# Performance work log

Hardware: AMD Instinct MI355X
Metric: run time of the kernel (lower is better)

## Reference

```python
import jax, jax.numpy as jnp
import numpy as np

NU, NI, NA = 100000, 50000, 5000
FEAT, H, L = 256, 128, 2
E_RATES, E_SIM, E_HAS = 1000000, 500000, 250000
SCALE = 0.05


def setup_inputs() -> dict:
    key = jax.random.key(0)
    ks = jax.random.split(key, 20)
    f32 = jnp.float32
    inp = {}
    inp["x_item_feat"] = jax.random.normal(ks[0], (NI, FEAT), f32)
    inp["user_emb"] = jax.random.normal(ks[1], (NU, H), f32) * SCALE
    inp["attr_emb"] = jax.random.normal(ks[2], (NA, H), f32) * SCALE
    inp["lin_item_W"] = jax.random.normal(ks[3], (FEAT, H), f32) * SCALE
    inp["lin_item_b"] = jnp.zeros((H,), f32)
    inp["ui_Wl"] = jax.random.normal(ks[4], (L, 4, H, H), f32) * SCALE
    inp["ui_bl"] = jnp.zeros((L, 4, H), f32)
    inp["ui_Wr"] = jax.random.normal(ks[5], (L, 4, H, H), f32) * SCALE
    inp["ii_Wl"] = jax.random.normal(ks[6], (L, 2, H, H), f32) * SCALE
    inp["ii_bl"] = jnp.zeros((L, 2, H), f32)
    inp["ii_Wr"] = jax.random.normal(ks[7], (L, 2, H, H), f32) * SCALE
    inp["ia_Wl"] = jax.random.normal(ks[8], (L, 4, H, H), f32) * SCALE
    inp["ia_bl"] = jnp.zeros((L, 4, H), f32)
    inp["ia_Wr"] = jax.random.normal(ks[9], (L, 4, H, H), f32) * SCALE
    inp["alpha"] = jnp.zeros((3,), f32)
    # edge_index rows: [src; dst], ranges per node type
    inp["edge_rates"] = jnp.stack([
        jax.random.randint(ks[10], (E_RATES,), 0, NU, jnp.int32),   # user src
        jax.random.randint(ks[11], (E_RATES,), 0, NI, jnp.int32)])  # item dst
    inp["edge_sim"] = jnp.stack([
        jax.random.randint(ks[12], (E_SIM,), 0, NI, jnp.int32),
        jax.random.randint(ks[13], (E_SIM,), 0, NI, jnp.int32)])
    inp["edge_has"] = jnp.stack([
        jax.random.randint(ks[14], (E_HAS,), 0, NI, jnp.int32),    # item src
        jax.random.randint(ks[15], (E_HAS,), 0, NA, jnp.int32)])   # attr dst
    return inp


def _sage_edge(x_src, x_dst, src, dst, Wl, bl, Wr):
    # PyG SAGEConv: lin_l(mean of neighbor messages) + lin_r(root)
    n_dst = x_dst.shape[0]
    agg = jax.ops.segment_sum(x_src[src], dst, num_segments=n_dst)
    cnt = jax.ops.segment_sum(jnp.ones(src.shape[0], x_src.dtype), dst, num_segments=n_dst)
    agg = agg / jnp.maximum(cnt, 1.0)[:, None]
    return agg @ Wl + bl + x_dst @ Wr


def _sage_self(x, Wl, bl, Wr):
    # 'self' relation realized as identity self-loops: mean aggr of single self neighbor = x
    return x @ Wl + bl + x @ Wr


def reference(x_item_feat, user_emb, attr_emb, lin_item_W, lin_item_b,
              ui_Wl, ui_bl, ui_Wr, ii_Wl, ii_bl, ii_Wr, ia_Wl, ia_bl, ia_Wr,
              alpha, edge_rates, edge_sim, edge_has):
    x_item = x_item_feat @ lin_item_W + lin_item_b
    relu = jax.nn.relu

    # user-item branch (relations: 0=rates u->i, 1=rev_rates i->u, 2=user self, 3=item self)
    hu, hi = user_emb, x_item
    for l in range(L):
        o_i = 0.5 * (_sage_edge(hu, hi, edge_rates[0], edge_rates[1], ui_Wl[l, 0], ui_bl[l, 0], ui_Wr[l, 0])
                     + _sage_self(hi, ui_Wl[l, 3], ui_bl[l, 3], ui_Wr[l, 3]))
        o_u = 0.5 * (_sage_edge(hi, hu, edge_rates[1], edge_rates[0], ui_Wl[l, 1], ui_bl[l, 1], ui_Wr[l, 1])
                     + _sage_self(hu, ui_Wl[l, 2], ui_bl[l, 2], ui_Wr[l, 2]))
        hu, hi = relu(o_u), relu(o_i)
    h_ui_item = hi

    # item-item content branch (0=sim, 1=item self)
    h = x_item
    for l in range(L):
        o = 0.5 * (_sage_edge(h, h, edge_sim[0], edge_sim[1], ii_Wl[l, 0], ii_bl[l, 0], ii_Wr[l, 0])
                   + _sage_self(h, ii_Wl[l, 1], ii_bl[l, 1], ii_Wr[l, 1]))
        h = relu(o)
    h_ii_item = h

    # item-attr branch (0=has i->a, 1=rev_has a->i, 2=item self, 3=attr self)
    hi2, ha = x_item, attr_emb
    for l in range(L):
        o_a = 0.5 * (_sage_edge(hi2, ha, edge_has[0], edge_has[1], ia_Wl[l, 0], ia_bl[l, 0], ia_Wr[l, 0])
                     + _sage_self(ha, ia_Wl[l, 3], ia_bl[l, 3], ia_Wr[l, 3]))
        o_i = 0.5 * (_sage_edge(ha, hi2, edge_has[1], edge_has[0], ia_Wl[l, 1], ia_bl[l, 1], ia_Wr[l, 1])
                     + _sage_self(hi2, ia_Wl[l, 2], ia_bl[l, 2], ia_Wr[l, 2]))
        hi2, ha = relu(o_i), relu(o_a)
    h_ia_item = hi2

    w = jax.nn.softmax(alpha)
    h_fused = w[0] * h_ui_item + w[1] * h_ii_item + w[2] * h_ia_item
    return (h_fused, h_ui_item, h_ii_item, h_ia_item, w)
```

## Files before the change

### kernel.cpp

```cpp
#include <hip/hip_runtime.h>

#define NU_ 100000
#define NI_ 50000
#define NA_ 5000
#define FEAT_ 256
#define H_ 128
#define ER_ 1000000
#define ES_ 500000
#define EH_ 250000

#define NTOT_ (3 * NI_ + NU_ + NA_)
#define RTOT_ (2 * ER_ + ES_ + 2 * EH_)
#define NSB_ ((NTOT_ + 1023) / 1024)
#define SBCAP_ 65536
#define B_RI 0
#define B_RU (NI_)
#define B_SI (NI_ + NU_)
#define B_HA (2 * NI_ + NU_)
#define B_HI (2 * NI_ + NU_ + NA_)

typedef long long i64;
typedef unsigned short u16;
typedef unsigned int u32;
typedef __attribute__((ext_vector_type(8))) short bf16x8;
typedef __attribute__((ext_vector_type(4))) float f32x4;

__device__ __forceinline__ u16 f2bf(float v) {
    u32 b = __float_as_uint(v);
    b += 0x7fff + ((b >> 16) & 1);
    return (u16)(b >> 16);
}
__device__ __forceinline__ float bf2f(u16 v) {
    return __uint_as_float((u32)v << 16);
}

__global__ __launch_bounds__(256) void tobf_kernel(const float4* __restrict__ in,
                                                   ushort4* __restrict__ out, long n4) {
    long i = (long)blockIdx.x * 256 + threadIdx.x;
    if (i >= n4) return;
    float4 v = in[i];
    ushort4 o;
    o.x = f2bf(v.x); o.y = f2bf(v.y); o.z = f2bf(v.z); o.w = f2bf(v.w);
    out[i] = o;
}

__device__ __forceinline__ void rec_of(int r, const int* __restrict__ er,
                                       const int* __restrict__ es,
                                       const int* __restrict__ eh,
                                       int& node, int& val) {
    if (r < 2 * ER_) {
        int e = r >> 1;
        if ((r & 1) == 0) { node = B_RI + er[ER_ + e]; val = er[e]; }
        else              { node = B_RU + er[e];       val = er[ER_ + e]; }
    } else if (r < 2 * ER_ + ES_) {
        int e = r - 2 * ER_;
        node = B_SI + es[ES_ + e]; val = es[e];
    } else {
        int q = r - 2 * ER_ - ES_;
        int e = q >> 1;
        if ((q & 1) == 0) { node = B_HA + eh[EH_ + e]; val = eh[e]; }
        else              { node = B_HI + eh[e];       val = eh[EH_ + e]; }
    }
}

__global__ __launch_bounds__(256) void sbinit_kernel(int* __restrict__ sbc,
                                                     int* __restrict__ OFF) {
    int t = threadIdx.x;
    sbc[t] = t << 16;
    if (t < 4) OFF[t] = 0;
}

__global__ __launch_bounds__(256) void binA_kernel(const int* __restrict__ er,
                                                   const int* __restrict__ es,
                                                   const int* __restrict__ eh,
                                                   int* __restrict__ sbc,
                                                   int* __restrict__ cpool) {
    __shared__ int h[256];
    __shared__ int gof[256];
    int t = threadIdx.x;
    h[t] = 0;
    __syncthreads();
    int base = blockIdx.x * 4096;
    int sbs[16];
    u32 recs[16];
#pragma unroll
    for (int i = 0; i < 16; ++i) {
        int r = base + i * 256 + t;
        sbs[i] = -1;
        if (r < RTOT_) {
            int node, val;
            rec_of(r, er, es, eh, node, val);
            int sb = node >> 10;
            sbs[i] = sb;
            recs[i] = ((u32)(node & 1023) << 17) | (u32)val;
            atomicAdd(&h[sb], 1);
        }
    }
    __syncthreads();
    {
        int c = h[t];
        if (c > 0) gof[t] = atomicAdd(&sbc[t], c);
        h[t] = 0;
    }
    __syncthreads();
#pragma unroll
    for (int i = 0; i < 16; ++i) {
        if (sbs[i] >= 0) {
            int slot = atomicAdd(&h[sbs[i]], 1);
            cpool[gof[sbs[i]] + slot] = (int)recs[i];
        }
    }
}

__global__ __launch_bounds__(256) void sbscan_kernel(const int* __restrict__ sbc,
                                                     int* __restrict__ sbb) {
    int t = threadIdx.x;
    int v = (t < NSB_) ? (sbc[t] - (t << 16)) : 0;
    int incl = v;
    int lane = t & 63;
#pragma unroll
    for (int d = 1; d < 64; d <<= 1) {
        int u = __shfl_up(incl, d);
        if (lane >= d) incl += u;
    }
    __shared__ int wsum[4];
    if (lane == 63) wsum[t >> 6] = incl;
    __syncthreads();
    int wo = 0;
    for (int i = 0; i < (t >> 6); ++i) wo += wsum[i];
    if (t < NSB_) sbb[t] = wo + incl - v;
}

__global__ __launch_bounds__(1024) void binB_kernel(const int* __restrict__ cpool,
                                                    const int* __restrict__ sbb,
                                                    const int* __restrict__ sbc,
                                                    int* __restrict__ off1,
                                                    int* __restrict__ pool) {
    __shared__ int c[1024];
    __shared__ int b[1024];
    __shared__ int wsum[16];
    int sb = blockIdx.x, t = threadIdx.x;
    int rlo = sb << 16, rhi = sbc[sb];
    int base = sbb[sb];
    c[t] = 0;
    __syncthreads();
    for (int j = rlo + t; j < rhi; j += 1024)
        atomicAdd(&c[((u32)cpool[j]) >> 17], 1);
    __syncthreads();
    int v = c[t];
    int incl = v;
    int lane = t & 63;
#pragma unroll
    for (int d = 1; d < 64; d <<= 1) {
        int u = __shfl_up(incl, d);
        if (lane >= d) incl += u;
    }
    if (lane == 63) wsum[t >> 6] = incl;
    __syncthreads();
    int wo = 0;
    for (int i = 0; i < (t >> 6); ++i) wo += wsum[i];
    int ex = wo + incl - v;
    int node = sb * 1024 + t;
    if (node < NTOT_) off1[node] = base + ex + v;
    b[t] = base + ex;
    __syncthreads();
    for (int j = rlo + t; j < rhi; j += 1024) {
        u32 rec = (u32)cpool[j];
        int pos = atomicAdd(&b[rec >> 17], 1);
        pool[pos] = (int)(rec & 0x1FFFF);
    }
}

#define ACC8(A, V)                                                            \
    {                                                                         \
        A[0] += bf2f((u16)(V.x & 0xffff)); A[1] += bf2f((u16)(V.x >> 16));    \
        A[2] += bf2f((u16)(V.y & 0xffff)); A[3] += bf2f((u16)(V.y >> 16));    \
        A[4] += bf2f((u16)(V.z & 0xffff)); A[5] += bf2f((u16)(V.z >> 16));    \
        A[6] += bf2f((u16)(V.w & 0xffff)); A[7] += bf2f((u16)(V.w >> 16));    \
    }

__global__ __launch_bounds__(256) void gatherb_kernel(const u16* __restrict__ feat,
                                                      const int* __restrict__ off1,
                                                      const int* __restrict__ pool,
                                                      int n,
                                                      u16* __restrict__ agg) {
    int row = blockIdx.x * 16 + (threadIdx.x >> 4);
    if (row >= n) return;
    int lane = (threadIdx.x & 15) * 8;
    int start = off1[row - 1];
    int end = off1[row];
    float a0[8], a1[8], a2[8], a3[8];
#pragma unroll
    for (int k = 0; k < 8; ++k) { a0[k] = 0.f; a1[k] = 0.f; a2[k] = 0.f; a3[k] = 0.f; }
    int j = start;
    for (; j + 4 <= end; j += 4) {
        int s0 = pool[j], s1 = pool[j + 1], s2 = pool[j + 2], s3 = pool[j + 3];
        uint4 v0 = *(const uint4*)&feat[(i64)s0 * H_ + lane];
        uint4 v1 = *(const uint4*)&feat[(i64)s1 * H_ + lane];
        uint4 v2 = *(const uint4*)&feat[(i64)s2 * H_ + lane];
        uint4 v3 = *(const uint4*)&feat[(i64)s3 * H_ + lane];
        ACC8(a0, v0); ACC8(a1, v1); ACC8(a2, v2); ACC8(a3, v3);
    }
    for (; j < end; ++j) {
        int s0 = pool[j];
        uint4 v0 = *(const uint4*)&feat[(i64)s0 * H_ + lane];
        ACC8(a0, v0);
    }
    float inv = 1.0f / fmaxf((float)(end - start), 1.0f);
    uint4 o;
    float r0, r1;
    r0 = (a0[0] + a1[0] + a2[0] + a3[0]) * inv; r1 = (a0[1] + a1[1] + a2[1] + a3[1]) * inv;
    o.x = (u32)f2bf(r0) | ((u32)f2bf(r1) << 16);
    r0 = (a0[2] + a1[2] + a2[2] + a3[2]) * inv; r1 = (a0[3] + a1[3] + a2[3] + a3[3]) * inv;
    o.y = (u32)f2bf(r0) | ((u32)f2bf(r1) << 16);
    r0 = (a0[4] + a1[4] + a2[4] + a3[4]) * inv; r1 = (a0[5] + a1[5] + a2[5] + a3[5]) * inv;
    o.z = (u32)f2bf(r0) | ((u32)f2bf(r1) << 16);
    r0 = (a0[6] + a1[6] + a2[6] + a3[6]) * inv; r1 = (a0[7] + a1[7] + a2[7] + a3[7]) * inv;
    o.w = (u32)f2bf(r0) | ((u32)f2bf(r1) << 16);
    *(uint4*)&agg[(i64)row * H_ + lane] = o;
}

struct WJob {
    const float* s0; const float* s1; const float* s2;
    int logK; int base;
};
struct WJobs { WJob j[17]; };

__global__ __launch_bounds__(256) void wsplit_kernel(WJobs jobs, int njobs, int total,
                                                     u16* __restrict__ WTH,
                                                     u16* __restrict__ WTL) {
    int gid = blockIdx.x * 256 + threadIdx.x;
    if (gid >= total) return;
    int ji = 0;
    for (int i = 1; i < 17; ++i)
        if (i < njobs && gid >= jobs.j[i].base) ji = i;
    WJob jb = jobs.j[ji];
    int local = gid - jb.base;
    int e = local & 7;
    int l = (local >> 3) & 63;
    int nt = (local >> 9) & 7;
    int kc = local >> 12;
    int n = nt * 16 + (l & 15);
    int k = kc * 32 + ((l >> 4) << 3) + e;
    i64 si = (i64)k * 128 + n;
    float v = jb.s0[si];
    if (jb.s1 != nullptr) v += jb.s1[si] + jb.s2[si];
    if (jb.logK == 8) {
        u32 b = __float_as_uint(v);
        u16 h = (u16)(b >> 16);
        float rem = v - __uint_as_float(b & 0xffff0000u);
        WTH[gid] = h;
        WTL[gid] = (u16)(__float_as_uint(rem) >> 16);
    } else {
        WTH[gid] = f2bf(v);
    }
}

__device__ __forceinline__ void split8(const float* f, bf16x8& h, bf16x8& lo) {
#pragma unroll
    for (int i = 0; i < 8; ++i) {
        u32 b = __float_as_uint(f[i]);
        h[i] = (short)(u16)(b >> 16);
        float rem = f[i] - __uint_as_float(b & 0xffff0000u);
        lo[i] = (short)(u16)(__float_as_uint(rem) >> 16);
    }
}

__global__ __launch_bounds__(256) void mgemm_x_kernel(
    const float* __restrict__ A, const u16* __restrict__ Wh, const u16* __restrict__ Wl,
    const float* __restrict__ bias, u16* __restrict__ Cbf, int M) {
    int t = threadIdx.x;
    int w = t >> 6, l = t & 63;
    int lr = l & 15, lq = l >> 4;
    int m0 = blockIdx.x * 128 + w * 32;

    f32x4 acc[2][8];
#pragma unroll
    for (int mt = 0; mt < 2; ++mt)
#pragma unroll
        for (int nt = 0; nt < 8; ++nt) acc[mt][nt] = (f32x4){0.f, 0.f, 0.f, 0.f};

    for (int kc = 0; kc < 8; ++kc) {
        bf16x8 ah0, al0, ah1, al1;
        {
            int row = m0 + lr;
            float f[8];
            if (row < M) {
                const float* ap = &A[(i64)row * FEAT_ + kc * 32 + lq * 8];
                *(float4*)&f[0] = *(const float4*)ap;
                *(float4*)&f[4] = *(const float4*)(ap + 4);
            } else {
#pragma unroll
                for (int i = 0; i < 8; ++i) f[i] = 0.f;
            }
            split8(f, ah0, al0);
        }
        {
            int row = m0 + 16 + lr;
            float f[8];
            if (row < M) {
                const float* ap = &A[(i64)row * FEAT_ + kc * 32 + lq * 8];
                *(float4*)&f[0] = *(const float4*)ap;
                *(float4*)&f[4] = *(const float4*)(ap + 4);
            } else {
#pragma unroll
                for (int i = 0; i < 8; ++i) f[i] = 0.f;
            }
            split8(f, ah1, al1);
        }
        const u16* whp = Wh + ((i64)kc * 8) * 512 + (i64)l * 8;
        const u16* wlp = Wl + ((i64)kc * 8) * 512 + (i64)l * 8;
#pragma unroll
        for (int nt = 0; nt < 8; ++nt) {
            bf16x8 bh = *(const bf16x8*)(whp + nt * 512);
            bf16x8 bl = *(const bf16x8*)(wlp + nt * 512);
            acc[0][nt] = __builtin_amdgcn_mfma_f32_16x16x32_bf16(ah0, bh, acc[0][nt], 0, 0, 0);
            acc[1][nt] = __builtin_amdgcn_mfma_f32_16x16x32_bf16(ah1, bh, acc[1][nt], 0, 0, 0);
            acc[0][nt] = __builtin_amdgcn_mfma_f32_16x16x32_bf16(al0, bh, acc[0][nt], 0, 0, 0);
            acc[1][nt] = __builtin_amdgcn_mfma_f32_16x16x32_bf16(al1, bh, acc[1][nt], 0, 0, 0);
            acc[0][nt] = __builtin_amdgcn_mfma_f32_16x16x32_bf16(ah0, bl, acc[0][nt], 0, 0, 0);
            acc[1][nt] = __builtin_amdgcn_mfma_f32_16x16x32_bf16(ah1, bl, acc[1][nt], 0, 0, 0);
        }
    }
#pragma unroll
    for (int nt = 0; nt < 8; ++nt) {
        int col = nt * 16 + lr;
        float bb = bias[col];
#pragma unroll
        for (int mt = 0; mt < 2; ++mt) {
#pragma unroll
            for (int r = 0; r < 4; ++r) {
                int row = m0 + mt * 16 + (lq << 2) + r;
                if (row < M) Cbf[(i64)row * H_ + col] = f2bf(acc[mt][nt][r] + bb);
            }
        }
    }
}

__global__ __launch_bounds__(256) void mgemm_d_kernel(
    const u16* __restrict__ A1, const u16* __restrict__ W1,
    const u16* __restrict__ A2, const u16* __restrict__ W2,
    const float* __restrict__ b1, const float* __restrict__ b2,
    float* __restrict__ C, u16* __restrict__ Cbf, int M,
    const float* __restrict__ alpha, const float* __restrict__ fu,
    const float* __restrict__ fi, float* __restrict__ fout,
    float* __restrict__ wout) {
    int t = threadIdx.x;
    int w = t >> 6, l = t & 63;
    int lr = l & 15, lq = l >> 4;
    int m0 = blockIdx.x * 128 + w * 32;

    f32x4 acc[2][8];
#pragma unroll
    for (int mt = 0; mt < 2; ++mt)
#pragma unroll
        for (int nt = 0; nt < 8; ++nt) acc[mt][nt] = (f32x4){0.f, 0.f, 0.f, 0.f};

#pragma unroll
    for (int mat = 0; mat < 2; ++mat) {
        const u16* A = mat ? A2 : A1;
        const u16* W = mat ? W2 : W1;
#pragma unroll
        for (int kc = 0; kc < 4; ++kc) {
            bf16x8 a0 = {0, 0, 0, 0, 0, 0, 0, 0}, a1 = {0, 0, 0, 0, 0, 0, 0, 0};
            int row0 = m0 + lr, row1 = m0 + 16 + lr;
            if (row0 < M) a0 = *(const bf16x8*)&A[(i64)row0 * H_ + kc * 32 + lq * 8];
            if (row1 < M) a1 = *(const bf16x8*)&A[(i64)row1 * H_ + kc * 32 + lq * 8];
            const u16* wp = W + ((i64)kc * 8) * 512 + (i64)l * 8;
#pragma unroll
            for (int nt = 0; nt < 8; ++nt) {
                bf16x8 bw = *(const bf16x8*)(wp + nt * 512);
                acc[0][nt] = __builtin_amdgcn_mfma_f32_16x16x32_bf16(a0, bw, acc[0][nt], 0, 0, 0);
                acc[1][nt] = __builtin_amdgcn_mfma_f32_16x16x32_bf16(a1, bw, acc[1][nt], 0, 0, 0);
            }
        }
    }

    float w0 = 0.f, w1 = 0.f, w2 = 0.f;
    if (fout != nullptr) {
        float x0 = alpha[0], x1 = alpha[1], x2 = alpha[2];
        float mx = fmaxf(x0, fmaxf(x1, x2));
        float e0 = __expf(x0 - mx), e1 = __expf(x1 - mx), e2 = __expf(x2 - mx);
        float inv = 1.f / (e0 + e1 + e2);
        w0 = e0 * inv; w1 = e1 * inv; w2 = e2 * inv;
        if (blockIdx.x == 0 && t == 0) { wout[0] = w0; wout[1] = w1; wout[2] = w2; }
    }

#pragma unroll
    for (int nt = 0; nt < 8; ++nt) {
        int col = nt * 16 + lr;
        float bb = 0.5f * (b1[col] + b2[col]);
#pragma unroll
        for (int mt = 0; mt < 2; ++mt) {
#pragma unroll
            for (int r = 0; r < 4; ++r) {
                int row = m0 + mt * 16 + (lq << 2) + r;
                if (row < M) {
                    i64 idx = (i64)row * H_ + col;
                    float o = fmaxf(0.5f * acc[mt][nt][r] + bb, 0.f);
                    if (C != nullptr) C[idx] = o;
                    if (Cbf != nullptr) Cbf[idx] = f2bf(o);
                    if (fout != nullptr) fout[idx] = w0 * fu[idx] + w1 * fi[idx] + w2 * o;
                }
            }
        }
    }
}

extern "C" void kernel_launch(void* const* d_in, const int* in_sizes, int n_in,
                              void* d_out, int out_size, void* d_ws, size_t ws_size,
                              hipStream_t stream) {
    const float* xif  = (const float*)d_in[0];
    const float* uemb = (const float*)d_in[1];
    const float* aemb = (const float*)d_in[2];
    const float* liW  = (const float*)d_in[3];
    const float* lib  = (const float*)d_in[4];
    const float* uiWl = (const float*)d_in[5];
    const float* uibl = (const float*)d_in[6];
    const float* uiWr = (const float*)d_in[7];
    const float* iiWl = (const float*)d_in[8];
    const float* iibl = (const float*)d_in[9];
    const float* iiWr = (const float*)d_in[10];
    const float* iaWl = (const float*)d_in[11];
    const float* iabl = (const float*)d_in[12];
    const float* iaWr = (const float*)d_in[13];
    const float* alpha = (const float*)d_in[14];
    const int* er = (const int*)d_in[15];
    const int* es = (const int*)d_in[16];
    const int* eh = (const int*)d_in[17];

    float* out = (float*)d_out;
    float* FUSED  = out;
    float* OUT_UI = out + (i64)NI_ * H_;
    float* OUT_II = out + (i64)2 * NI_ * H_;
    float* OUT_IA = out + (i64)3 * NI_ * H_;
    float* WOUT   = out + (i64)4 * NI_ * H_;

    u16* u = (u16*)d_ws;
    i64 uo = 0;
    u16* WTH    = u + uo; uo += 294912;
    u16* WTL    = u + uo; uo += 294912;
    u16* X_bf   = u + uo; uo += (i64)NI_ * H_;
    u16* HI1_bf = u + uo; uo += (i64)NI_ * H_;
    u16* HU1_bf = u + uo; uo += (i64)NU_ * H_;
    u16* HA1_bf = u + uo; uo += (i64)NA_ * H_;
    u16* AGG_bf = u + uo; uo += (i64)NU_ * H_;
    u16* UE_bf  = u + uo; uo += (i64)NU_ * H_;
    u16* AE_bf  = u + uo; uo += (i64)NA_ * H_;

    int* ip = (int*)(u + uo);
    i64 io = 0;
    int* OFF   = ip + io; io += NTOT_ + 4;
    int* SBB   = ip + io; io += 256;
    int* SBC   = ip + io; io += 256;
    int* POOL  = ip + io; io += RTOT_;
    int* CPOOL = ip + io; io += (i64)NSB_ << 16;
    int* off1 = OFF + 1;

    {
        sbinit_kernel<<<1, 256, 0, stream>>>(SBC, OFF);
        int nblk = (RTOT_ + 4095) / 4096;
        binA_kernel<<<nblk, 256, 0, stream>>>(er, es, eh, SBC, CPOOL);
        sbscan_kernel<<<1, 256, 0, stream>>>(SBC, SBB);
        binB_kernel<<<NSB_, 1024, 0, stream>>>(CPOOL, SBB, SBC, off1, POOL);
    }

    const float* famWl[8] = {uiWl, uiWl, uiWl, iiWl, iiWl, iaWl, iaWl, iaWl};
    const float* famWr[8] = {uiWr, uiWr, uiWr, iiWr, iiWr, iaWr, iaWr, iaWr};
    const float* famBl[8] = {uibl, uibl, uibl, iibl, iibl, iabl, iabl, iabl};
    const int eidx[8] = {0, 1, 4, 0, 2, 0, 1, 5};
    const int sidx[8] = {3, 2, 7, 1, 3, 3, 2, 6};

    WJobs jobs;
    jobs.j[0] = {liW, nullptr, nullptr, 8, 0};
    int base = 32768;
    for (int s = 0; s < 8; ++s) {
        jobs.j[1 + 2 * s] = {famWl[s] + (i64)eidx[s] * 16384, nullptr, nullptr, 7, base};
        base += 16384;
        jobs.j[2 + 2 * s] = {famWr[s] + (i64)eidx[s] * 16384,
                             famWl[s] + (i64)sidx[s] * 16384,
                             famWr[s] + (i64)sidx[s] * 16384, 7, base};
        base += 16384;
    }
    wsplit_kernel<<<(base + 255) / 256, 256, 0, stream>>>(jobs, 17, base, WTH, WTL);

    tobf_kernel<<<((NU_ * H_ / 4) + 255) / 256, 256, 0, stream>>>(
        (const float4*)uemb, (ushort4*)UE_bf, (long)NU_ * H_ / 4);
    tobf_kernel<<<((NA_ * H_ / 4) + 255) / 256, 256, 0, stream>>>(
        (const float4*)aemb, (ushort4*)AE_bf, (long)NA_ * H_ / 4);

    mgemm_x_kernel<<<(NI_ + 127) / 128, 256, 0, stream>>>(xif, WTH, WTL, lib, X_bf, NI_);

    auto gath = [&](const u16* feat, int cbase, int ndst) {
        gatherb_kernel<<<(ndst + 15) / 16, 256, 0, stream>>>(feat, off1 + cbase, POOL, ndst, AGG_bf);
    };
    auto gemm2 = [&](int slot, const u16* A2m, float* Cout, u16* Cbfout, int M,
                     const float* al = nullptr, const float* fu = nullptr,
                     const float* fi = nullptr, float* fo = nullptr,
                     float* wo = nullptr) {
        const u16* w1 = WTH + 32768 + (i64)(2 * slot) * 16384;
        const u16* w2 = WTH + 32768 + (i64)(2 * slot + 1) * 16384;
        const float* be = famBl[slot] + (i64)eidx[slot] * 128;
        const float* bs = famBl[slot] + (i64)sidx[slot] * 128;
        mgemm_d_kernel<<<(M + 127) / 128, 256, 0, stream>>>(
            AGG_bf, w1, A2m, w2, be, bs, Cout, Cbfout, M, al, fu, fi, fo, wo);
    };

    gath(UE_bf, B_RI, NI_);
    gemm2(0, X_bf, nullptr, HI1_bf, NI_);
    gath(X_bf, B_RU, NU_);
    gemm2(1, UE_bf, nullptr, HU1_bf, NU_);
    gath(HU1_bf, B_RI, NI_);
    gemm2(2, HI1_bf, OUT_UI, nullptr, NI_);

    gath(X_bf, B_SI, NI_);
    gemm2(3, X_bf, nullptr, HI1_bf, NI_);
    gath(HI1_bf, B_SI, NI_);
    gemm2(4, HI1_bf, OUT_II, nullptr, NI_);

    gath(X_bf, B_HA, NA_);
    gemm2(5, AE_bf, nullptr, HA1_bf, NA_);
    gath(AE_bf, B_HI, NI_);
    gemm2(6, X_bf, nullptr, HI1_bf, NI_);
    gath(HA1_bf, B_HI, NI_);
    gemm2(7, HI1_bf, OUT_IA, nullptr, NI_, alpha, OUT_UI, OUT_II, FUSED, WOUT);
}
```

Before: 549.7 us.

## Batch independent gather and GEMM stages into packed multi-op launches

Replaces the serial chain of 17 gather/GEMM kernel launches with 6 launches of a packed kernel. Each launch runs several independent operations from the three branches concurrently, and the block index is dispatched to the op it belongs to. Separate aggregation and hidden buffers per branch remove the false dependencies that the shared AGG/HI1 buffers forced. This is meant to cut launch overhead and fill the GPU during small stages. In exchange it uses more workspace memory and a single kernel with larger register pressure across the combined code paths.

```diff
diff --git a/kernel.cpp b/kernel.cpp
--- a/kernel.cpp
+++ b/kernel.cpp
@@ -12,7 +12,6 @@
 #define NTOT_ (3 * NI_ + NU_ + NA_)
 #define RTOT_ (2 * ER_ + ES_ + 2 * EH_)
 #define NSB_ ((NTOT_ + 1023) / 1024)
-#define SBCAP_ 65536
 #define B_RI 0
 #define B_RU (NI_)
 #define B_SI (NI_ + NU_)
@@ -169,55 +168,6 @@
         int pos = atomicAdd(&b[rec >> 17], 1);
         pool[pos] = (int)(rec & 0x1FFFF);
     }
-}
-
-#define ACC8(A, V)                                                            \
-    {                                                                         \
-        A[0] += bf2f((u16)(V.x & 0xffff)); A[1] += bf2f((u16)(V.x >> 16));    \
-        A[2] += bf2f((u16)(V.y & 0xffff)); A[3] += bf2f((u16)(V.y >> 16));    \
-        A[4] += bf2f((u16)(V.z & 0xffff)); A[5] += bf2f((u16)(V.z >> 16));    \
-        A[6] += bf2f((u16)(V.w & 0xffff)); A[7] += bf2f((u16)(V.w >> 16));    \
-    }
-
-__global__ __launch_bounds__(256) void gatherb_kernel(const u16* __restrict__ feat,
-                                                      const int* __restrict__ off1,
-                                                      const int* __restrict__ pool,
-                                                      int n,
-                                                      u16* __restrict__ agg) {
-    int row = blockIdx.x * 16 + (threadIdx.x >> 4);
-    if (row >= n) return;
-    int lane = (threadIdx.x & 15) * 8;
-    int start = off1[row - 1];
-    int end = off1[row];
-    float a0[8], a1[8], a2[8], a3[8];
-#pragma unroll
-    for (int k = 0; k < 8; ++k) { a0[k] = 0.f; a1[k] = 0.f; a2[k] = 0.f; a3[k] = 0.f; }
-    int j = start;
-    for (; j + 4 <= end; j += 4) {
-        int s0 = pool[j], s1 = pool[j + 1], s2 = pool[j + 2], s3 = pool[j + 3];
-        uint4 v0 = *(const uint4*)&feat[(i64)s0 * H_ + lane];
-        uint4 v1 = *(const uint4*)&feat[(i64)s1 * H_ + lane];
-        uint4 v2 = *(const uint4*)&feat[(i64)s2 * H_ + lane];
-        uint4 v3 = *(const uint4*)&feat[(i64)s3 * H_ + lane];
-        ACC8(a0, v0); ACC8(a1, v1); ACC8(a2, v2); ACC8(a3, v3);
-    }
-    for (; j < end; ++j) {
-        int s0 = pool[j];
-        uint4 v0 = *(const uint4*)&feat[(i64)s0 * H_ + lane];
-        ACC8(a0, v0);
-    }
-    float inv = 1.0f / fmaxf((float)(end - start), 1.0f);
-    uint4 o;
-    float r0, r1;
-    r0 = (a0[0] + a1[0] + a2[0] + a3[0]) * inv; r1 = (a0[1] + a1[1] + a2[1] + a3[1]) * inv;
-    o.x = (u32)f2bf(r0) | ((u32)f2bf(r1) << 16);
-    r0 = (a0[2] + a1[2] + a2[2] + a3[2]) * inv; r1 = (a0[3] + a1[3] + a2[3] + a3[3]) * inv;
-    o.y = (u32)f2bf(r0) | ((u32)f2bf(r1) << 16);
-    r0 = (a0[4] + a1[4] + a2[4] + a3[4]) * inv; r1 = (a0[5] + a1[5] + a2[5] + a3[5]) * inv;
-    o.z = (u32)f2bf(r0) | ((u32)f2bf(r1) << 16);
-    r0 = (a0[6] + a1[6] + a2[6] + a3[6]) * inv; r1 = (a0[7] + a1[7] + a2[7] + a3[7]) * inv;
-    o.w = (u32)f2bf(r0) | ((u32)f2bf(r1) << 16);
-    *(uint4*)&agg[(i64)row * H_ + lane] = o;
 }
 
 struct WJob {
@@ -256,6 +206,54 @@
     }
 }
 
+#define ACC8(A, V)                                                            \
+    {                                                                         \
+        A[0] += bf2f((u16)(V.x & 0xffff)); A[1] += bf2f((u16)(V.x >> 16));    \
+        A[2] += bf2f((u16)(V.y & 0xffff)); A[3] += bf2f((u16)(V.y >> 16));    \
+        A[4] += bf2f((u16)(V.z & 0xffff)); A[5] += bf2f((u16)(V.z >> 16));    \
+        A[6] += bf2f((u16)(V.w & 0xffff)); A[7] += bf2f((u16)(V.w >> 16));    \
+    }
+
+__device__ void gather_dev(int b, const u16* __restrict__ feat,
+                           const int* __restrict__ off1c,
+                           const int* __restrict__ pool, int n,
+                           u16* __restrict__ agg) {
+    int row = b * 16 + (threadIdx.x >> 4);
+    if (row >= n) return;
+    int lane = (threadIdx.x & 15) * 8;
+    int start = off1c[row - 1];
+    int end = off1c[row];
+    float a0[8], a1[8], a2[8], a3[8];
+#pragma unroll
+    for (int k = 0; k < 8; ++k) { a0[k] = 0.f; a1[k] = 0.f; a2[k] = 0.f; a3[k] = 0.f; }
+    int j = start;
+    for (; j + 4 <= end; j += 4) {
+        int s0 = pool[j], s1 = pool[j + 1], s2 = pool[j + 2], s3 = pool[j + 3];
+        uint4 v0 = *(const uint4*)&feat[(i64)s0 * H_ + lane];
+        uint4 v1 = *(const uint4*)&feat[(i64)s1 * H_ + lane];
+        uint4 v2 = *(const uint4*)&feat[(i64)s2 * H_ + lane];
+        uint4 v3 = *(const uint4*)&feat[(i64)s3 * H_ + lane];
+        ACC8(a0, v0); ACC8(a1, v1); ACC8(a2, v2); ACC8(a3, v3);
+    }
+    for (; j < end; ++j) {
+        int s0 = pool[j];
+        uint4 v0 = *(const uint4*)&feat[(i64)s0 * H_ + lane];
+        ACC8(a0, v0);
+    }
+    float inv = 1.0f / fmaxf((float)(end - start), 1.0f);
+    uint4 o;
+    float r0, r1;
+    r0 = (a0[0] + a1[0] + a2[0] + a3[0]) * inv; r1 = (a0[1] + a1[1] + a2[1] + a3[1]) * inv;
+    o.x = (u32)f2bf(r0) | ((u32)f2bf(r1) << 16);
+    r0 = (a0[2] + a1[2] + a2[2] + a3[2]) * inv; r1 = (a0[3] + a1[3] + a2[3] + a3[3]) * inv;
+    o.y = (u32)f2bf(r0) | ((u32)f2bf(r1) << 16);
+    r0 = (a0[4] + a1[4] + a2[4] + a3[4]) * inv; r1 = (a0[5] + a1[5] + a2[5] + a3[5]) * inv;
+    o.z = (u32)f2bf(r0) | ((u32)f2bf(r1) << 16);
+    r0 = (a0[6] + a1[6] + a2[6] + a3[6]) * inv; r1 = (a0[7] + a1[7] + a2[7] + a3[7]) * inv;
+    o.w = (u32)f2bf(r0) | ((u32)f2bf(r1) << 16);
+    *(uint4*)&agg[(i64)row * H_ + lane] = o;
+}
+
 __device__ __forceinline__ void split8(const float* f, bf16x8& h, bf16x8& lo) {
 #pragma unroll
     for (int i = 0; i < 8; ++i) {
@@ -266,13 +264,13 @@
     }
 }
 
-__global__ __launch_bounds__(256) void mgemm_x_kernel(
-    const float* __restrict__ A, const u16* __restrict__ Wh, const u16* __restrict__ Wl,
-    const float* __restrict__ bias, u16* __restrict__ Cbf, int M) {
+__device__ void xgemm_dev(int blk, const float* __restrict__ A,
+                          const u16* __restrict__ Wh, const u16* __restrict__ Wl,
+                          const float* __restrict__ bias, u16* __restrict__ Cbf, int M) {
     int t = threadIdx.x;
     int w = t >> 6, l = t & 63;
     int lr = l & 15, lq = l >> 4;
-    int m0 = blockIdx.x * 128 + w * 32;
+    int m0 = blk * 128 + w * 32;
 
     f32x4 acc[2][8];
 #pragma unroll
@@ -337,18 +335,17 @@
     }
 }
 
-__global__ __launch_bounds__(256) void mgemm_d_kernel(
-    const u16* __restrict__ A1, const u16* __restrict__ W1,
-    const u16* __restrict__ A2, const u16* __restrict__ W2,
-    const float* __restrict__ b1, const float* __restrict__ b2,
-    float* __restrict__ C, u16* __restrict__ Cbf, int M,
-    const float* __restrict__ alpha, const float* __restrict__ fu,
-    const float* __restrict__ fi, float* __restrict__ fout,
-    float* __restrict__ wout) {
+__device__ void gemm_dev(int blk, const u16* __restrict__ A1, const u16* __restrict__ W1,
+                         const u16* __restrict__ A2, const u16* __restrict__ W2,
+                         const float* __restrict__ b1, const float* __restrict__ b2,
+                         float* __restrict__ C, u16* __restrict__ Cbf, int M,
+                         bool dofuse, const float* __restrict__ alpha,
+                         const float* __restrict__ fu, const float* __restrict__ fi,
+                         float* __restrict__ fout, float* __restrict__ wout) {
     int t = threadIdx.x;
     int w = t >> 6, l = t & 63;
     int lr = l & 15, lq = l >> 4;
-    int m0 = blockIdx.x * 128 + w * 32;
+    int m0 = blk * 128 + w * 32;
 
     f32x4 acc[2][8];
 #pragma unroll
@@ -377,13 +374,13 @@
     }
 
     float w0 = 0.f, w1 = 0.f, w2 = 0.f;
-    if (fout != nullptr) {
+    if (dofuse) {
         float x0 = alpha[0], x1 = alpha[1], x2 = alpha[2];
         float mx = fmaxf(x0, fmaxf(x1, x2));
         float e0 = __expf(x0 - mx), e1 = __expf(x1 - mx), e2 = __expf(x2 - mx);
         float inv = 1.f / (e0 + e1 + e2);
         w0 = e0 * inv; w1 = e1 * inv; w2 = e2 * inv;
-        if (blockIdx.x == 0 && t == 0) { wout[0] = w0; wout[1] = w1; wout[2] = w2; }
+        if (blk == 0 && t == 0) { wout[0] = w0; wout[1] = w1; wout[2] = w2; }
     }
 
 #pragma unroll
@@ -400,10 +397,43 @@
                     float o = fmaxf(0.5f * acc[mt][nt][r] + bb, 0.f);
                     if (C != nullptr) C[idx] = o;
                     if (Cbf != nullptr) Cbf[idx] = f2bf(o);
-                    if (fout != nullptr) fout[idx] = w0 * fu[idx] + w1 * fi[idx] + w2 * o;
+                    if (dofuse) fout[idx] = w0 * fu[idx] + w1 * fi[idx] + w2 * o;
                 }
             }
         }
+    }
+}
+
+struct Op {
+    const void* p0; const void* p1; const void* p2; const void* p3;
+    const void* p4; const void* p5;
+    void* q0; void* q1;
+    int kind;
+    int nblk;
+    int n;
+    int pad;
+};
+struct Ops { Op op[5]; };
+
+__global__ __launch_bounds__(256) void packed_kernel(
+    Ops ops, int nops, const int* __restrict__ pool,
+    const float* __restrict__ alpha, const float* __restrict__ fu,
+    const float* __restrict__ fi, float* __restrict__ fout,
+    float* __restrict__ wout) {
+    int b = blockIdx.x;
+    int i = 0;
+    while (i < nops - 1 && b >= ops.op[i].nblk) { b -= ops.op[i].nblk; ++i; }
+    Op o = ops.op[i];
+    if (o.kind == 0) {
+        gather_dev(b, (const u16*)o.p0, (const int*)o.p1, pool, o.n, (u16*)o.q0);
+    } else if (o.kind == 2) {
+        xgemm_dev(b, (const float*)o.p0, (const u16*)o.p1, (const u16*)o.p2,
+                  (const float*)o.p4, (u16*)o.q0, o.n);
+    } else {
+        gemm_dev(b, (const u16*)o.p0, (const u16*)o.p1, (const u16*)o.p2,
+                 (const u16*)o.p3, (const float*)o.p4, (const float*)o.p5,
+                 (float*)o.q0, (u16*)o.q1, o.n, o.kind == 3,
+                 alpha, fu, fi, fout, wout);
     }
 }
 
@@ -441,12 +471,21 @@
     u16* WTH    = u + uo; uo += 294912;
     u16* WTL    = u + uo; uo += 294912;
     u16* X_bf   = u + uo; uo += (i64)NI_ * H_;
-    u16* HI1_bf = u + uo; uo += (i64)NI_ * H_;
+    u16* HIU_bf = u + uo; uo += (i64)NI_ * H_;
+    u16* HII_bf = u + uo; uo += (i64)NI_ * H_;
+    u16* HIA_bf = u + uo; uo += (i64)NI_ * H_;
     u16* HU1_bf = u + uo; uo += (i64)NU_ * H_;
     u16* HA1_bf = u + uo; uo += (i64)NA_ * H_;
-    u16* AGG_bf = u + uo; uo += (i64)NU_ * H_;
     u16* UE_bf  = u + uo; uo += (i64)NU_ * H_;
     u16* AE_bf  = u + uo; uo += (i64)NA_ * H_;
+    u16* AGG1 = u + uo; uo += (i64)NI_ * H_;
+    u16* AGG2 = u + uo; uo += (i64)NU_ * H_;
+    u16* AGG3 = u + uo; uo += (i64)NI_ * H_;
+    u16* AGG4 = u + uo; uo += (i64)NI_ * H_;
+    u16* AGG5 = u + uo; uo += (i64)NI_ * H_;
+    u16* AGG6 = u + uo; uo += (i64)NA_ * H_;
+    u16* AGG7 = u + uo; uo += (i64)NI_ * H_;
+    u16* AGG8 = u + uo; uo += (i64)NI_ * H_;
 
     int* ip = (int*)(u + uo);
     i64 io = 0;
@@ -489,39 +528,74 @@
     tobf_kernel<<<((NA_ * H_ / 4) + 255) / 256, 256, 0, stream>>>(
         (const float4*)aemb, (ushort4*)AE_bf, (long)NA_ * H_ / 4);
 
-    mgemm_x_kernel<<<(NI_ + 127) / 128, 256, 0, stream>>>(xif, WTH, WTL, lib, X_bf, NI_);
-
-    auto gath = [&](const u16* feat, int cbase, int ndst) {
-        gatherb_kernel<<<(ndst + 15) / 16, 256, 0, stream>>>(feat, off1 + cbase, POOL, ndst, AGG_bf);
+    auto mkgather = [&](const u16* feat, int cbase, int n, u16* agg) {
+        Op o{};
+        o.kind = 0; o.nblk = (n + 15) / 16; o.n = n;
+        o.p0 = feat; o.p1 = off1 + cbase; o.q0 = agg;
+        return o;
     };
-    auto gemm2 = [&](int slot, const u16* A2m, float* Cout, u16* Cbfout, int M,
-                     const float* al = nullptr, const float* fu = nullptr,
-                     const float* fi = nullptr, float* fo = nullptr,
-                     float* wo = nullptr) {
-        const u16* w1 = WTH + 32768 + (i64)(2 * slot) * 16384;
-        const u16* w2 = WTH + 32768 + (i64)(2 * slot + 1) * 16384;
-        const float* be = famBl[slot] + (i64)eidx[slot] * 128;
-        const float* bs = famBl[slot] + (i64)sidx[slot] * 128;
-        mgemm_d_kernel<<<(M + 127) / 128, 256, 0, stream>>>(
-            AGG_bf, w1, A2m, w2, be, bs, Cout, Cbfout, M, al, fu, fi, fo, wo);
+    auto mkgemm = [&](int slot, const u16* agg, const u16* A2, float* C, u16* Cbf,
+                      int M, int kind) {
+        Op o{};
+        o.kind = kind; o.nblk = (M + 127) / 128; o.n = M;
+        o.p0 = agg;
+        o.p1 = WTH + 32768 + (i64)(2 * slot) * 16384;
+        o.p2 = A2;
+        o.p3 = WTH + 32768 + (i64)(2 * slot + 1) * 16384;
+        o.p4 = famBl[slot] + (i64)eidx[slot] * 128;
+        o.p5 = famBl[slot] + (i64)sidx[slot] * 128;
+        o.q0 = C; o.q1 = Cbf;
+        return o;
     };
-
-    gath(UE_bf, B_RI, NI_);
-    gemm2(0, X_bf, nullptr, HI1_bf, NI_);
-    gath(X_bf, B_RU, NU_);
-    gemm2(1, UE_bf, nullptr, HU1_bf, NU_);
-    gath(HU1_bf, B_RI, NI_);
-    gemm2(2, HI1_bf, OUT_UI, nullptr, NI_);
-
-    gath(X_bf, B_SI, NI_);
-    gemm2(3, X_bf, nullptr, HI1_bf, NI_);
-    gath(HI1_bf, B_SI, NI_);
-    gemm2(4, HI1_bf, OUT_II, nullptr, NI_);
-
-    gath(X_bf, B_HA, NA_);
-    gemm2(5, AE_bf, nullptr, HA1_bf, NA_);
-    gath(AE_bf, B_HI, NI_);
-    gemm2(6, X_bf, nullptr, HI1_bf, NI_);
-    gath(HA1_bf, B_HI, NI_);
-    gemm2(7, HI1_bf, OUT_IA, nullptr, NI_, alpha, OUT_UI, OUT_II, FUSED, WOUT);
-}
+    auto launch = [&](Ops& ops, int nops) {
+        int grid = 0;
+        for (int i = 0; i < nops; ++i) grid += ops.op[i].nblk;
+        packed_kernel<<<grid, 256, 0, stream>>>(ops, nops, POOL, alpha,
+                                                OUT_UI, OUT_II, FUSED, WOUT);
+    };
+
+    {
+        Ops ops{};
+        Op ox{};
+        ox.kind = 2; ox.nblk = (NI_ + 127) / 128; ox.n = NI_;
+        ox.p0 = xif; ox.p1 = WTH; ox.p2 = WTL; ox.p4 = lib; ox.q0 = X_bf;
+        ops.op[0] = ox;
+        ops.op[1] = mkgather(UE_bf, B_RI, NI_, AGG1);
+        launch(ops, 2);
+    }
+    {
+        Ops ops{};
+        ops.op[0] = mkgemm(0, AGG1, X_bf, nullptr, HIU_bf, NI_, 1);
+        ops.op[1] = mkgather(X_bf, B_RU, NU_, AGG2);
+        ops.op[2] = mkgather(X_bf, B_SI, NI_, AGG4);
+        ops.op[3] = mkgather(X_bf, B_HA, NA_, AGG6);
+        ops.op[4] = mkgather(AE_bf, B_HI, NI_, AGG7);
+        launch(ops, 5);
+    }
+    {
+        Ops ops{};
+        ops.op[0] = mkgemm(1, AGG2, UE_bf, nullptr, HU1_bf, NU_, 1);
+        ops.op[1] = mkgemm(3, AGG4, X_bf, nullptr, HII_bf, NI_, 1);
+        ops.op[2] = mkgemm(5, AGG6, AE_bf, nullptr, HA1_bf, NA_, 1);
+        ops.op[3] = mkgemm(6, AGG7, X_bf, nullptr, HIA_bf, NI_, 1);
+        launch(ops, 4);
+    }
+    {
+        Ops ops{};
+        ops.op[0] = mkgather(HU1_bf, B_RI, NI_, AGG3);
+        ops.op[1] = mkgather(HII_bf, B_SI, NI_, AGG5);
+        ops.op[2] = mkgather(HA1_bf, B_HI, NI_, AGG8);
+        launch(ops, 3);
+    }
+    {
+        Ops ops{};
+        ops.op[0] = mkgemm(2, AGG3, HIU_bf, OUT_UI, nullptr, NI_, 1);
+        ops.op[1] = mkgemm(4, AGG5, HII_bf, OUT_II, nullptr, NI_, 1);
+        launch(ops, 2);
+    }
+    {
+        Ops ops{};
+        ops.op[0] = mkgemm(7, AGG8, HIA_bf, OUT_IA, nullptr, NI_, 3);
+        launch(ops, 1);
+    }
+}
```

New measurement: 624.4 us. 13.6% more time.

## Batch independent gathers and GEMMs across branches into packed launches

Applied to the files above, without the earlier changes.

Replaces the serial sequence of eight gather+GEMM pairs with grouped launches. Each packed kernel decodes its block index into an op table, so independent branch layers share one launch. Separate aggregation and hidden buffers per branch remove the reuse hazards that forced serialization. The two embedding bf16 conversions are also merged into one launch. This cuts launch count and the tail of small grids such as the attr ops, at the cost of more workspace memory and a small per-block op lookup.

```diff
diff --git a/kernel.cpp b/kernel.cpp
--- a/kernel.cpp
+++ b/kernel.cpp
@@ -12,7 +12,6 @@
 #define NTOT_ (3 * NI_ + NU_ + NA_)
 #define RTOT_ (2 * ER_ + ES_ + 2 * EH_)
 #define NSB_ ((NTOT_ + 1023) / 1024)
-#define SBCAP_ 65536
 #define B_RI 0
 #define B_RU (NI_)
 #define B_SI (NI_ + NU_)
@@ -34,14 +33,19 @@
     return __uint_as_float((u32)v << 16);
 }
 
-__global__ __launch_bounds__(256) void tobf_kernel(const float4* __restrict__ in,
-                                                   ushort4* __restrict__ out, long n4) {
+__global__ __launch_bounds__(256) void tobf2_kernel(const float4* __restrict__ inU,
+                                                    ushort4* __restrict__ outU, long n4u,
+                                                    const float4* __restrict__ inA,
+                                                    ushort4* __restrict__ outA, long n4a) {
     long i = (long)blockIdx.x * 256 + threadIdx.x;
-    if (i >= n4) return;
-    float4 v = in[i];
+    const float4* in; ushort4* out;
+    if (i < n4u) { in = inU + i; out = outU + i; }
+    else if (i < n4u + n4a) { in = inA + (i - n4u); out = outA + (i - n4u); }
+    else return;
+    float4 v = *in;
     ushort4 o;
     o.x = f2bf(v.x); o.y = f2bf(v.y); o.z = f2bf(v.z); o.w = f2bf(v.w);
-    out[i] = o;
+    *out = o;
 }
 
 __device__ __forceinline__ void rec_of(int r, const int* __restrict__ er,
@@ -169,55 +173,6 @@
         int pos = atomicAdd(&b[rec >> 17], 1);
         pool[pos] = (int)(rec & 0x1FFFF);
     }
-}
-
-#define ACC8(A, V)                                                            \
-    {                                                                         \
-        A[0] += bf2f((u16)(V.x & 0xffff)); A[1] += bf2f((u16)(V.x >> 16));    \
-        A[2] += bf2f((u16)(V.y & 0xffff)); A[3] += bf2f((u16)(V.y >> 16));    \
-        A[4] += bf2f((u16)(V.z & 0xffff)); A[5] += bf2f((u16)(V.z >> 16));    \
-        A[6] += bf2f((u16)(V.w & 0xffff)); A[7] += bf2f((u16)(V.w >> 16));    \
-    }
-
-__global__ __launch_bounds__(256) void gatherb_kernel(const u16* __restrict__ feat,
-                                                      const int* __restrict__ off1,
-                                                      const int* __restrict__ pool,
-                                                      int n,
-                                                      u16* __restrict__ agg) {
-    int row = blockIdx.x * 16 + (threadIdx.x >> 4);
-    if (row >= n) return;
-    int lane = (threadIdx.x & 15) * 8;
-    int start = off1[row - 1];
-    int end = off1[row];
-    float a0[8], a1[8], a2[8], a3[8];
-#pragma unroll
-    for (int k = 0; k < 8; ++k) { a0[k] = 0.f; a1[k] = 0.f; a2[k] = 0.f; a3[k] = 0.f; }
-    int j = start;
-    for (; j + 4 <= end; j += 4) {
-        int s0 = pool[j], s1 = pool[j + 1], s2 = pool[j + 2], s3 = pool[j + 3];
-        uint4 v0 = *(const uint4*)&feat[(i64)s0 * H_ + lane];
-        uint4 v1 = *(const uint4*)&feat[(i64)s1 * H_ + lane];
-        uint4 v2 = *(const uint4*)&feat[(i64)s2 * H_ + lane];
-        uint4 v3 = *(const uint4*)&feat[(i64)s3 * H_ + lane];
-        ACC8(a0, v0); ACC8(a1, v1); ACC8(a2, v2); ACC8(a3, v3);
-    }
-    for (; j < end; ++j) {
-        int s0 = pool[j];
-        uint4 v0 = *(const uint4*)&feat[(i64)s0 * H_ + lane];
-        ACC8(a0, v0);
-    }
-    float inv = 1.0f / fmaxf((float)(end - start), 1.0f);
-    uint4 o;
-    float r0, r1;
-    r0 = (a0[0] + a1[0] + a2[0] + a3[0]) * inv; r1 = (a0[1] + a1[1] + a2[1] + a3[1]) * inv;
-    o.x = (u32)f2bf(r0) | ((u32)f2bf(r1) << 16);
-    r0 = (a0[2] + a1[2] + a2[2] + a3[2]) * inv; r1 = (a0[3] + a1[3] + a2[3] + a3[3]) * inv;
-    o.y = (u32)f2bf(r0) | ((u32)f2bf(r1) << 16);
-    r0 = (a0[4] + a1[4] + a2[4] + a3[4]) * inv; r1 = (a0[5] + a1[5] + a2[5] + a3[5]) * inv;
-    o.z = (u32)f2bf(r0) | ((u32)f2bf(r1) << 16);
-    r0 = (a0[6] + a1[6] + a2[6] + a3[6]) * inv; r1 = (a0[7] + a1[7] + a2[7] + a3[7]) * inv;
-    o.w = (u32)f2bf(r0) | ((u32)f2bf(r1) << 16);
-    *(uint4*)&agg[(i64)row * H_ + lane] = o;
 }
 
 struct WJob {
@@ -256,6 +211,63 @@
     }
 }
 
+#define ACC8(A, V)                                                            \
+    {                                                                         \
+        A[0] += bf2f((u16)(V.x & 0xffff)); A[1] += bf2f((u16)(V.x >> 16));    \
+        A[2] += bf2f((u16)(V.y & 0xffff)); A[3] += bf2f((u16)(V.y >> 16));    \
+        A[4] += bf2f((u16)(V.z & 0xffff)); A[5] += bf2f((u16)(V.z >> 16));    \
+        A[6] += bf2f((u16)(V.w & 0xffff)); A[7] += bf2f((u16)(V.w >> 16));    \
+    }
+
+struct GOp {
+    const u16* feat; const int* off1c; u16* agg;
+    int nblk; int n; int pad0; int pad1; int pad2;
+};
+struct GOps { GOp op[5]; };
+
+__global__ __launch_bounds__(256) void packed_gather_kernel(GOps ops, int nops,
+                                                            const int* __restrict__ pool) {
+    int b = blockIdx.x;
+    int i = 0;
+    while (i < nops - 1 && b >= ops.op[i].nblk) { b -= ops.op[i].nblk; ++i; }
+    GOp o = ops.op[i];
+    int row = b * 16 + (threadIdx.x >> 4);
+    if (row >= o.n) return;
+    int lane = (threadIdx.x & 15) * 8;
+    int start = o.off1c[row - 1];
+    int end = o.off1c[row];
+    const u16* feat = o.feat;
+    float a0[8], a1[8], a2[8], a3[8];
+#pragma unroll
+    for (int k = 0; k < 8; ++k) { a0[k] = 0.f; a1[k] = 0.f; a2[k] = 0.f; a3[k] = 0.f; }
+    int j = start;
+    for (; j + 4 <= end; j += 4) {
+        int s0 = pool[j], s1 = pool[j + 1], s2 = pool[j + 2], s3 = pool[j + 3];
+        uint4 v0 = *(const uint4*)&feat[(i64)s0 * H_ + lane];
+        uint4 v1 = *(const uint4*)&feat[(i64)s1 * H_ + lane];
+        uint4 v2 = *(const uint4*)&feat[(i64)s2 * H_ + lane];
+        uint4 v3 = *(const uint4*)&feat[(i64)s3 * H_ + lane];
+        ACC8(a0, v0); ACC8(a1, v1); ACC8(a2, v2); ACC8(a3, v3);
+    }
+    for (; j < end; ++j) {
+        int s0 = pool[j];
+        uint4 v0 = *(const uint4*)&feat[(i64)s0 * H_ + lane];
+        ACC8(a0, v0);
+    }
+    float inv = 1.0f / fmaxf((float)(end - start), 1.0f);
+    uint4 o4;
+    float r0, r1;
+    r0 = (a0[0] + a1[0] + a2[0] + a3[0]) * inv; r1 = (a0[1] + a1[1] + a2[1] + a3[1]) * inv;
+    o4.x = (u32)f2bf(r0) | ((u32)f2bf(r1) << 16);
+    r0 = (a0[2] + a1[2] + a2[2] + a3[2]) * inv; r1 = (a0[3] + a1[3] + a2[3] + a3[3]) * inv;
+    o4.y = (u32)f2bf(r0) | ((u32)f2bf(r1) << 16);
+    r0 = (a0[4] + a1[4] + a2[4] + a3[4]) * inv; r1 = (a0[5] + a1[5] + a2[5] + a3[5]) * inv;
+    o4.z = (u32)f2bf(r0) | ((u32)f2bf(r1) << 16);
+    r0 = (a0[6] + a1[6] + a2[6] + a3[6]) * inv; r1 = (a0[7] + a1[7] + a2[7] + a3[7]) * inv;
+    o4.w = (u32)f2bf(r0) | ((u32)f2bf(r1) << 16);
+    *(uint4*)&o.agg[(i64)row * H_ + lane] = o4;
+}
+
 __device__ __forceinline__ void split8(const float* f, bf16x8& h, bf16x8& lo) {
 #pragma unroll
     for (int i = 0; i < 8; ++i) {
@@ -337,18 +349,28 @@
     }
 }
 
-__global__ __launch_bounds__(256) void mgemm_d_kernel(
-    const u16* __restrict__ A1, const u16* __restrict__ W1,
-    const u16* __restrict__ A2, const u16* __restrict__ W2,
-    const float* __restrict__ b1, const float* __restrict__ b2,
-    float* __restrict__ C, u16* __restrict__ Cbf, int M,
+struct MOp {
+    const u16* A1; const u16* W1; const u16* A2; const u16* W2;
+    const float* b1; const float* b2;
+    float* C; u16* Cbf;
+    int nblk; int n; int fuse; int pad;
+};
+struct MOps { MOp op[5]; };
+
+__global__ __launch_bounds__(256) void packed_gemm_kernel(
+    MOps ops, int nops,
     const float* __restrict__ alpha, const float* __restrict__ fu,
     const float* __restrict__ fi, float* __restrict__ fout,
     float* __restrict__ wout) {
+    int blk = blockIdx.x;
+    int i = 0;
+    while (i < nops - 1 && blk >= ops.op[i].nblk) { blk -= ops.op[i].nblk; ++i; }
+    MOp o = ops.op[i];
     int t = threadIdx.x;
     int w = t >> 6, l = t & 63;
     int lr = l & 15, lq = l >> 4;
-    int m0 = blockIdx.x * 128 + w * 32;
+    int m0 = blk * 128 + w * 32;
+    int M = o.n;
 
     f32x4 acc[2][8];
 #pragma unroll
@@ -358,8 +380,8 @@
 
 #pragma unroll
     for (int mat = 0; mat < 2; ++mat) {
-        const u16* A = mat ? A2 : A1;
-        const u16* W = mat ? W2 : W1;
+        const u16* A = mat ? o.A2 : o.A1;
+        const u16* W = mat ? o.W2 : o.W1;
 #pragma unroll
         for (int kc = 0; kc < 4; ++kc) {
             bf16x8 a0 = {0, 0, 0, 0, 0, 0, 0, 0}, a1 = {0, 0, 0, 0, 0, 0, 0, 0};
@@ -377,19 +399,19 @@
     }
 
     float w0 = 0.f, w1 = 0.f, w2 = 0.f;
-    if (fout != nullptr) {
+    if (o.fuse) {
         float x0 = alpha[0], x1 = alpha[1], x2 = alpha[2];
         float mx = fmaxf(x0, fmaxf(x1, x2));
         float e0 = __expf(x0 - mx), e1 = __expf(x1 - mx), e2 = __expf(x2 - mx);
         float inv = 1.f / (e0 + e1 + e2);
         w0 = e0 * inv; w1 = e1 * inv; w2 = e2 * inv;
-        if (blockIdx.x == 0 && t == 0) { wout[0] = w0; wout[1] = w1; wout[2] = w2; }
+        if (blk == 0 && t == 0) { wout[0] = w0; wout[1] = w1; wout[2] = w2; }
     }
 
 #pragma unroll
     for (int nt = 0; nt < 8; ++nt) {
         int col = nt * 16 + lr;
-        float bb = 0.5f * (b1[col] + b2[col]);
+        float bb = 0.5f * (o.b1[col] + o.b2[col]);
 #pragma unroll
         for (int mt = 0; mt < 2; ++mt) {
 #pragma unroll
@@ -397,10 +419,10 @@
                 int row = m0 + mt * 16 + (lq << 2) + r;
                 if (row < M) {
                     i64 idx = (i64)row * H_ + col;
-                    float o = fmaxf(0.5f * acc[mt][nt][r] + bb, 0.f);
-                    if (C != nullptr) C[idx] = o;
-                    if (Cbf != nullptr) Cbf[idx] = f2bf(o);
-                    if (fout != nullptr) fout[idx] = w0 * fu[idx] + w1 * fi[idx] + w2 * o;
+                    float v = fmaxf(0.5f * acc[mt][nt][r] + bb, 0.f);
+                    if (o.C != nullptr) o.C[idx] = v;
+                    if (o.Cbf != nullptr) o.Cbf[idx] = f2bf(v);
+                    if (o.fuse) fout[idx] = w0 * fu[idx] + w1 * fi[idx] + w2 * v;
                 }
             }
         }
@@ -441,12 +463,21 @@
     u16* WTH    = u + uo; uo += 294912;
     u16* WTL    = u + uo; uo += 294912;
     u16* X_bf   = u + uo; uo += (i64)NI_ * H_;
-    u16* HI1_bf = u + uo; uo += (i64)NI_ * H_;
+    u16* HIU_bf = u + uo; uo += (i64)NI_ * H_;
+    u16* HII_bf = u + uo; uo += (i64)NI_ * H_;
+    u16* HIA_bf = u + uo; uo += (i64)NI_ * H_;
     u16* HU1_bf = u + uo; uo += (i64)NU_ * H_;
     u16* HA1_bf = u + uo; uo += (i64)NA_ * H_;
-    u16* AGG_bf = u + uo; uo += (i64)NU_ * H_;
     u16* UE_bf  = u + uo; uo += (i64)NU_ * H_;
     u16* AE_bf  = u + uo; uo += (i64)NA_ * H_;
+    u16* AGG1 = u + uo; uo += (i64)NI_ * H_;
+    u16* AGG2 = u + uo; uo += (i64)NU_ * H_;
+    u16* AGG3 = u + uo; uo += (i64)NI_ * H_;
+    u16* AGG4 = u + uo; uo += (i64)NI_ * H_;
+    u16* AGG5 = u + uo; uo += (i64)NI_ * H_;
+    u16* AGG6 = u + uo; uo += (i64)NA_ * H_;
+    u16* AGG7 = u + uo; uo += (i64)NI_ * H_;
+    u16* AGG8 = u + uo; uo += (i64)NI_ * H_;
 
     int* ip = (int*)(u + uo);
     i64 io = 0;
@@ -484,44 +515,78 @@
     }
     wsplit_kernel<<<(base + 255) / 256, 256, 0, stream>>>(jobs, 17, base, WTH, WTL);
 
-    tobf_kernel<<<((NU_ * H_ / 4) + 255) / 256, 256, 0, stream>>>(
-        (const float4*)uemb, (ushort4*)UE_bf, (long)NU_ * H_ / 4);
-    tobf_kernel<<<((NA_ * H_ / 4) + 255) / 256, 256, 0, stream>>>(
-        (const float4*)aemb, (ushort4*)AE_bf, (long)NA_ * H_ / 4);
+    long n4u = (long)NU_ * H_ / 4, n4a = (long)NA_ * H_ / 4;
+    tobf2_kernel<<<(int)((n4u + n4a + 255) / 256), 256, 0, stream>>>(
+        (const float4*)uemb, (ushort4*)UE_bf, n4u,
+        (const float4*)aemb, (ushort4*)AE_bf, n4a);
 
     mgemm_x_kernel<<<(NI_ + 127) / 128, 256, 0, stream>>>(xif, WTH, WTL, lib, X_bf, NI_);
 
-    auto gath = [&](const u16* feat, int cbase, int ndst) {
-        gatherb_kernel<<<(ndst + 15) / 16, 256, 0, stream>>>(feat, off1 + cbase, POOL, ndst, AGG_bf);
+    auto mkg = [&](const u16* feat, int cbase, int n, u16* agg) {
+        GOp o{};
+        o.feat = feat; o.off1c = off1 + cbase; o.agg = agg;
+        o.nblk = (n + 15) / 16; o.n = n;
+        return o;
     };
-    auto gemm2 = [&](int slot, const u16* A2m, float* Cout, u16* Cbfout, int M,
-                     const float* al = nullptr, const float* fu = nullptr,
-                     const float* fi = nullptr, float* fo = nullptr,
-                     float* wo = nullptr) {
-        const u16* w1 = WTH + 32768 + (i64)(2 * slot) * 16384;
-        const u16* w2 = WTH + 32768 + (i64)(2 * slot + 1) * 16384;
-        const float* be = famBl[slot] + (i64)eidx[slot] * 128;
-        const float* bs = famBl[slot] + (i64)sidx[slot] * 128;
-        mgemm_d_kernel<<<(M + 127) / 128, 256, 0, stream>>>(
-            AGG_bf, w1, A2m, w2, be, bs, Cout, Cbfout, M, al, fu, fi, fo, wo);
+    auto glaunch = [&](GOps& ops, int nops) {
+        int grid = 0;
+        for (int i = 0; i < nops; ++i) grid += ops.op[i].nblk;
+        packed_gather_kernel<<<grid, 256, 0, stream>>>(ops, nops, POOL);
     };
-
-    gath(UE_bf, B_RI, NI_);
-    gemm2(0, X_bf, nullptr, HI1_bf, NI_);
-    gath(X_bf, B_RU, NU_);
-    gemm2(1, UE_bf, nullptr, HU1_bf, NU_);
-    gath(HU1_bf, B_RI, NI_);
-    gemm2(2, HI1_bf, OUT_UI, nullptr, NI_);
-
-    gath(X_bf, B_SI, NI_);
-    gemm2(3, X_bf, nullptr, HI1_bf, NI_);
-    gath(HI1_bf, B_SI, NI_);
-    gemm2(4, HI1_bf, OUT_II, nullptr, NI_);
-
-    gath(X_bf, B_HA, NA_);
-    gemm2(5, AE_bf, nullptr, HA1_bf, NA_);
-    gath(AE_bf, B_HI, NI_);
-    gemm2(6, X_bf, nullptr, HI1_bf, NI_);
-    gath(HA1_bf, B_HI, NI_);
-    gemm2(7, HI1_bf, OUT_IA, nullptr, NI_, alpha, OUT_UI, OUT_II, FUSED, WOUT);
-}
+    auto mkm = [&](int slot, const u16* agg, const u16* A2, float* C, u16* Cbf,
+                   int M, int fuse) {
+        MOp o{};
+        o.A1 = agg;
+        o.W1 = WTH + 32768 + (i64)(2 * slot) * 16384;
+        o.A2 = A2;
+        o.W2 = WTH + 32768 + (i64)(2 * slot + 1) * 16384;
+        o.b1 = famBl[slot] + (i64)eidx[slot] * 128;
+        o.b2 = famBl[slot] + (i64)sidx[slot] * 128;
+        o.C = C; o.Cbf = Cbf;
+        o.nblk = (M + 127) / 128; o.n = M; o.fuse = fuse;
+        return o;
+    };
+    auto mlaunch = [&](MOps& ops, int nops) {
+        int grid = 0;
+        for (int i = 0; i < nops; ++i) grid += ops.op[i].nblk;
+        packed_gemm_kernel<<<grid, 256, 0, stream>>>(ops, nops, alpha,
+                                                     OUT_UI, OUT_II, FUSED, WOUT);
+    };
+
+    {
+        GOps g{};
+        g.op[0] = mkg(X_bf, B_HA, NA_, AGG6);
+        g.op[1] = mkg(UE_bf, B_RI, NI_, AGG1);
+        g.op[2] = mkg(X_bf, B_RU, NU_, AGG2);
+        g.op[3] = mkg(X_bf, B_SI, NI_, AGG4);
+        g.op[4] = mkg(AE_bf, B_HI, NI_, AGG7);
+        glaunch(g, 5);
+    }
+    {
+        MOps m{};
+        m.op[0] = mkm(1, AGG2, UE_bf, nullptr, HU1_bf, NU_, 0);
+        m.op[1] = mkm(0, AGG1, X_bf, nullptr, HIU_bf, NI_, 0);
+        m.op[2] = mkm(3, AGG4, X_bf, nullptr, HII_bf, NI_, 0);
+        m.op[3] = mkm(6, AGG7, X_bf, nullptr, HIA_bf, NI_, 0);
+        m.op[4] = mkm(5, AGG6, AE_bf, nullptr, HA1_bf, NA_, 0);
+        mlaunch(m, 5);
+    }
+    {
+        GOps g{};
+        g.op[0] = mkg(HU1_bf, B_RI, NI_, AGG3);
+        g.op[1] = mkg(HII_bf, B_SI, NI_, AGG5);
+        g.op[2] = mkg(HA1_bf, B_HI, NI_, AGG8);
+        glaunch(g, 3);
+    }
+    {
+        MOps m{};
+        m.op[0] = mkm(2, AGG3, HIU_bf, OUT_UI, nullptr, NI_, 0);
+        m.op[1] = mkm(4, AGG5, HII_bf, OUT_II, nullptr, NI_, 0);
+        mlaunch(m, 2);
+    }
+    {
+        MOps m{};
+        m.op[0] = mkm(7, AGG8, HIA_bf, OUT_IA, nullptr, NI_, 1);
+        mlaunch(m, 1);
+    }
+}
```

Result: faster. 498.1 us (-9.4%).
